# Performance work log

Hardware: AMD Instinct MI355X
Metric: run time of the kernel (lower is better)

Reference implementation:

```python
import jax, jax.numpy as jnp
import numpy as np

B, T, DIM, HEADS, DH = 4, 2048, 1024, 16, 64
MAX_SEQ_LEN = 2048


def setup_inputs() -> dict:
    key = jax.random.key(0)
    k1, k2, k3, k4 = jax.random.split(key, 4)
    x = jax.random.normal(k1, (B, T, DIM), dtype=jnp.float32)
    W_qkv = jax.random.normal(k2, (DIM, 3 * HEADS * DH), dtype=jnp.float32) * (DIM ** -0.5)
    W_0 = jax.random.normal(k3, (HEADS * DH, DIM), dtype=jnp.float32) * ((HEADS * DH) ** -0.5)
    rel_bias = jax.random.normal(k4, (2 * MAX_SEQ_LEN - 1, HEADS), dtype=jnp.float32) * 0.02
    return {"x": x, "W_qkv": W_qkv, "W_0": W_0, "rel_bias": rel_bias}


def reference(x, W_qkv, W_0, rel_bias):
    b, t, dim = x.shape
    heads = rel_bias.shape[1]
    dh = W_qkv.shape[1] // (3 * heads)
    scale = dh ** -0.5

    qkv = x @ W_qkv  # (b, t, 3*heads*dh), feature layout is (d, k, h): d slowest, h fastest
    qkv = qkv.reshape(b, t, dh, 3, heads)
    qkv = jnp.transpose(qkv, (3, 0, 4, 1, 2))  # (3, b, h, t, d)
    q, k, v = qkv[0], qkv[1], qkv[2]

    scores = jnp.einsum('bhid,bhjd->bhij', q, k) * scale  # (b, h, t, t)

    causal = jnp.tril(jnp.ones((t, t), dtype=bool))
    scores = jnp.where(causal[None, None], scores, -jnp.inf)

    # relative position bias: index = j - i + t - 1
    rel_idx = jnp.arange(t)[None, :] - jnp.arange(t)[:, None] + (t - 1)  # (t, t)
    bias = rel_bias[rel_idx]  # (t, t, heads)
    scores = scores + jnp.transpose(bias, (2, 0, 1))[None]

    attn = jax.nn.softmax(scores, axis=-1)
    out = jnp.einsum('bhij,bhjd->bhid', attn, v)  # (b, h, t, d)
    out = jnp.transpose(out, (0, 2, 1, 3)).reshape(b, t, heads * dh)
    return out @ W_0
```

## Files before the change

### kernel.cpp

```cpp
#include <hip/hip_runtime.h>
#include <hip/hip_bf16.h>
#include <stdint.h>

#define B_ 4
#define T_ 2048
#define NH 16
#define DH 64
#define DIM 1024
#define NF 3072
#define QKS 2048

typedef unsigned short u16;
typedef uint32_t u32;
typedef __bf16 bf16;
typedef bf16 bf16x8 __attribute__((ext_vector_type(8)));
typedef float f32x4 __attribute__((ext_vector_type(4)));
typedef u16 u16x8 __attribute__((ext_vector_type(8)));
typedef u16 u16x4 __attribute__((ext_vector_type(4)));

__device__ __forceinline__ u16 f2bf(float f) {
    u32 u = __builtin_bit_cast(u32, f);
    u = (u + 0x7fffu + ((u >> 16) & 1u)) >> 16;
    return (u16)u;
}

__device__ __forceinline__ float exp2f_fast(float x) {
#if __has_builtin(__builtin_amdgcn_exp2f)
    return __builtin_amdgcn_exp2f(x);
#else
    return exp2f(x);
#endif
}

#define GLOAD16(g, l)                                                          \
    __builtin_amdgcn_global_load_lds(                                          \
        (const __attribute__((address_space(1))) u32*)(g),                     \
        (__attribute__((address_space(3))) u32*)(l), 16, 0, 0)


__global__ __launch_bounds__(256) void cvt_bf16_k(const float* __restrict__ src,
                                                  u16* __restrict__ dst, int n8) {
    int i = blockIdx.x * 256 + threadIdx.x;
    if (i >= n8) return;
    const float4* s = (const float4*)src + (size_t)i * 2;
    float4 a = s[0], b = s[1];
    u16x8 o;
    o[0]=f2bf(a.x); o[1]=f2bf(a.y); o[2]=f2bf(a.z); o[3]=f2bf(a.w);
    o[4]=f2bf(b.x); o[5]=f2bf(b.y); o[6]=f2bf(b.z); o[7]=f2bf(b.w);
    *(u16x8*)(dst + (size_t)i * 8) = o;
}

template <int PERM>
__global__ __launch_bounds__(256) void wcvt_t_k(const float* __restrict__ src,
                                                u16* __restrict__ dst, int K, int N) {
    __shared__ float tile[32][33];
    int n0 = blockIdx.x * 32, k0 = blockIdx.y * 32;
    int c = threadIdx.x & 31, r0 = threadIdx.x >> 5;
#pragma unroll
    for (int i = 0; i < 4; i++) {
        int r = r0 + i * 8;
        tile[r][c] = src[(size_t)(k0 + r) * N + n0 + c];
    }
    __syncthreads();
#pragma unroll
    for (int i = 0; i < 4; i++) {
        int r = r0 + i * 8;
        int n = n0 + r;
        int nd;
        if (PERM) {
            int d = n / 48, rem = n - d * 48;
            int kk = rem >> 4, h = rem & 15;
            nd = kk * 1024 + h * 64 + d;
        } else {
            nd = n;
        }
        dst[(size_t)nd * K + k0 + c] = f2bf(tile[c][r]);
    }
}

__global__ __launch_bounds__(256) void rbt_k(const float* __restrict__ rb,
                                             u16* __restrict__ rbT2,
                                             u16* __restrict__ rbT2s) {
    int i = blockIdx.x * 256 + threadIdx.x;
    if (i >= NH * 4096) return;
    int h = i >> 12, d = i & 4095;
    float v = (d <= 2047) ? rb[(size_t)d * NH + h] * 1.44269504f : -1e30f;
    rbT2[i] = __builtin_bit_cast(u16, (bf16)v);
    int d2 = d + 1;
    float v2 = (d2 <= 2047) ? rb[(size_t)d2 * NH + h] * 1.44269504f : -1e30f;
    rbT2s[i] = __builtin_bit_cast(u16, (bf16)v2);
}


template <int OUTMODE>
__global__ __launch_bounds__(256, 2) void gemm_bt_k(const u16* __restrict__ A,
                                                    const u16* __restrict__ Bt,
                                                    void* __restrict__ Cout,
                                                    u16* __restrict__ Vt,
                                                    int M, int N, int K) {
    __shared__ __align__(16) u16 As[128 * 64];
    __shared__ __align__(16) u16 Bs[128 * 64];
    const int tid = threadIdx.x;
    const int wave = tid >> 6, lane = tid & 63;
    const int bm = blockIdx.x, bn = blockIdx.y;
    const int wr = (wave >> 1) * 64, wc = (wave & 1) * 64;
    const int lrow = lane & 15, g4 = lane >> 4;
    const int srow8 = lane >> 3;
    const int scs = (lane & 7) ^ srow8;
    const u16* Ab = A + (size_t)(bm * 128 + wave * 32) * K;
    const u16* Bb = Bt + (size_t)(bn * 128 + wave * 32) * K;
    u16* AsW = As + wave * 2048;
    u16* BsW = Bs + wave * 2048;
    const bool vt = (OUTMODE == 1) && (bn >= 16);
    f32x4 acc[4][4] = {};

    for (int k0 = 0; k0 < K; k0 += 64) {
        __syncthreads();
#pragma unroll
        for (int g = 0; g < 4; g++) {
            GLOAD16(Ab + (size_t)(g * 8 + srow8) * K + k0 + scs * 8, AsW + g * 512);
            GLOAD16(Bb + (size_t)(g * 8 + srow8) * K + k0 + scs * 8, BsW + g * 512);
        }
        __syncthreads();
#pragma unroll
        for (int kk2 = 0; kk2 < 2; kk2++) {
            bf16x8 af[4], bfr[4];
#pragma unroll
            for (int i = 0; i < 4; i++)
                af[i] = *(const bf16x8*)&As[(wr + i * 16 + lrow) * 64 +
                                            (((kk2 * 4 + g4) ^ (lrow & 7)) * 8)];
#pragma unroll
            for (int j = 0; j < 4; j++)
                bfr[j] = *(const bf16x8*)&Bs[(wc + j * 16 + lrow) * 64 +
                                             (((kk2 * 4 + g4) ^ (lrow & 7)) * 8)];
            if (vt) {
#pragma unroll
                for (int i = 0; i < 4; i++)
#pragma unroll
                    for (int j = 0; j < 4; j++)
                        acc[i][j] = __builtin_amdgcn_mfma_f32_16x16x32_bf16(
                            bfr[j], af[i], acc[i][j], 0, 0, 0);
            } else {
#pragma unroll
                for (int i = 0; i < 4; i++)
#pragma unroll
                    for (int j = 0; j < 4; j++)
                        acc[i][j] = __builtin_amdgcn_mfma_f32_16x16x32_bf16(
                            af[i], bfr[j], acc[i][j], 0, 0, 0);
            }
        }
    }

    const int crow = (lane >> 4) * 4, ccol = lane & 15;
    if (vt) {
#pragma unroll
        for (int i = 0; i < 4; i++)
#pragma unroll
            for (int j = 0; j < 4; j++) {
                int gm = bm * 128 + wr + i * 16 + ccol;
                int b = gm >> 11, tt = gm & 2047;
#pragma unroll
                for (int r = 0; r < 4; r++) {
                    int f = (bn - 16) * 128 + wc + j * 16 + crow + r;
                    int h = f >> 6, d = f & 63;
                    Vt[(((size_t)(b * NH + h)) * DH + d) * T_ + tt] =
                        f2bf(acc[i][j][r]);
                }
            }
    } else {
#pragma unroll
        for (int i = 0; i < 4; i++)
#pragma unroll
            for (int j = 0; j < 4; j++) {
                int gm = bm * 128 + wr + i * 16 + crow;
                int gn = bn * 128 + wc + j * 16 + ccol;
#pragma unroll
                for (int r = 0; r < 4; r++) {
                    if (OUTMODE == 1)
                        ((u16*)Cout)[(size_t)(gm + r) * N + gn] = f2bf(acc[i][j][r]);
                    else
                        ((float*)Cout)[(size_t)(gm + r) * N + gn] = acc[i][j][r];
                }
            }
    }
}

__global__ __launch_bounds__(256, 2) void flash_attn_k(const u16* __restrict__ qkF,
                                                       const u16* __restrict__ Vt,
                                                       const u16* __restrict__ rbT2,
                                                       const u16* __restrict__ rbT2s,
                                                       u16* __restrict__ O) {
    __shared__ __align__(16) u16 Ks[2][64 * 64];
    __shared__ __align__(16) u16 Vs[2][64 * 64];
    __shared__ __align__(16) u16 Ps[4][2][16 * 64];
    __shared__ __align__(16) u16 rbs2a[4096];
    __shared__ __align__(16) u16 rbs2b[4096];
    const int tid = threadIdx.x, wave = tid >> 6, lane = tid & 63;
    const int Lid = blockIdx.x;
    const int c = Lid & 7, u = Lid >> 3;
    const int bh = ((u & 7) << 3) | c;
    const int pair = u >> 3;
    const int h = bh & 15, b = bh >> 4;
    const int l15 = lane & 15, g4 = lane >> 4;
    const float SC2 = 0.125f * 1.44269504f;

    {
        *(u16x8*)&rbs2a[tid * 8] = *(const u16x8*)&rbT2[(size_t)h * 4096 + tid * 8];
        *(u16x8*)&rbs2a[2048 + tid * 8] = *(const u16x8*)&rbT2[(size_t)h * 4096 + 2048 + tid * 8];
        *(u16x8*)&rbs2b[tid * 8] = *(const u16x8*)&rbT2s[(size_t)h * 4096 + tid * 8];
        *(u16x8*)&rbs2b[2048 + tid * 8] = *(const u16x8*)&rbT2s[(size_t)h * 4096 + 2048 + tid * 8];
    }

    const size_t trow = (size_t)b * T_;
    u16* pwA = &Ps[wave][0][0];
    u16* pwB = &Ps[wave][1][0];
    const int lrow8 = lane >> 3, lch = lane & 7;
    const int swz = lch ^ lrow8;
    const u16* kg0 = &qkF[(trow + wave * 16 + lrow8) * QKS + 1024 + h * 64 + swz * 8];
    const u16* kg1 = kg0 + (size_t)8 * QKS;
    const u16* vg0 = &Vt[((size_t)bh * DH + wave * 16 + lrow8) * T_ + swz * 8];
    const u16* vg1 = vg0 + (size_t)8 * T_;

#define STAGE_KV(j0n, buf)                                                     \
    do {                                                                       \
        GLOAD16(kg0 + (size_t)(j0n) * QKS, &Ks[buf][(wave * 16) * 64]);        \
        GLOAD16(kg1 + (size_t)(j0n) * QKS, &Ks[buf][(wave * 16 + 8) * 64]);    \
        GLOAD16(vg0 + (j0n), &Vs[buf][(wave * 16) * 64]);                      \
        GLOAD16(vg1 + (j0n), &Vs[buf][(wave * 16 + 8) * 64]);                  \
    } while (0)

    STAGE_KV(0, 0);
    __syncthreads();
    int cur = 0;

    for (int half = 0; half < 2; half++) {
        const int blk = half ? 15 - pair : pair;
        const int qbA = blk * 128 + wave * 16;
        const int qbB = qbA + 64;
        bf16x8 aqA[2], aqB[2];
        aqA[0] = *(const bf16x8*)&qkF[(trow + qbA + l15) * QKS + h * 64 + g4 * 8];
        aqA[1] = *(const bf16x8*)&qkF[(trow + qbA + l15) * QKS + h * 64 + 32 + g4 * 8];
        aqB[0] = *(const bf16x8*)&qkF[(trow + qbB + l15) * QKS + h * 64 + g4 * 8];
        aqB[1] = *(const bf16x8*)&qkF[(trow + qbB + l15) * QKS + h * 64 + 32 + g4 * 8];

        const int ibA = 2047 - l15 + g4 * 4 - qbA;
        const u32* b32A = (const u32*)((ibA & 1) ? &rbs2b[ibA - 1] : &rbs2a[ibA]);
        const u32* b32B = b32A - 32;

        f32x4 oaccA[4] = {}, oaccB[4] = {};
        float lA = 0.f, lB = 0.f;

        const int jtmax = 2 * blk + 1;
        for (int jt = 0; jt <= jtmax; jt++) {
            const int j0 = jt * 64;
            const int j0n = (jt + 1 <= jtmax) ? (jt + 1) * 64 : (half == 0 ? 0 : -1);
            if (j0n >= 0) STAGE_KV(j0n, cur ^ 1);
            const u16* KsC = &Ks[cur][0];
            const u16* VsC = &Vs[cur][0];
            f32x4 sA[4], sB[4];
#pragma unroll
            for (int ni = 0; ni < 4; ni++) {
                f32x4 z = {};
                sA[ni] = z;
                sB[ni] = z;
            }
            __builtin_amdgcn_s_setprio(1);
#pragma unroll
            for (int ni = 0; ni < 4; ni++) {
                int arow = ni * 16 + l15;
#pragma unroll
                for (int kk = 0; kk < 2; kk++) {
                    int ch = kk * 4 + g4;
                    bf16x8 ak = *(const bf16x8*)&KsC[arow * 64 + ((ch ^ (arow & 7)) * 8)];
                    sA[ni] = __builtin_amdgcn_mfma_f32_16x16x32_bf16(ak, aqA[kk], sA[ni], 0, 0, 0);
                    sB[ni] = __builtin_amdgcn_mfma_f32_16x16x32_bf16(ak, aqB[kk], sB[ni], 0, 0, 0);
                }
            }
            __builtin_amdgcn_s_setprio(0);
            const int jo = j0 >> 1;
            {
                float su = 0.f;
#pragma unroll
                for (int ni = 0; ni < 4; ni++) {
                    u32 w0 = b32A[jo + ni * 8];
                    u32 w1 = b32A[jo + ni * 8 + 1];
                    float e0 = exp2f_fast(fmaf(sA[ni][0], SC2, __builtin_bit_cast(float, w0 << 16)));
                    float e1 = exp2f_fast(fmaf(sA[ni][1], SC2, __builtin_bit_cast(float, w0 & 0xffff0000u)));
                    float e2 = exp2f_fast(fmaf(sA[ni][2], SC2, __builtin_bit_cast(float, w1 << 16)));
                    float e3 = exp2f_fast(fmaf(sA[ni][3], SC2, __builtin_bit_cast(float, w1 & 0xffff0000u)));
                    su += (e0 + e1) + (e2 + e3);
                    u16x4 pk;
                    pk[0] = __builtin_bit_cast(u16, (bf16)e0);
                    pk[1] = __builtin_bit_cast(u16, (bf16)e1);
                    pk[2] = __builtin_bit_cast(u16, (bf16)e2);
                    pk[3] = __builtin_bit_cast(u16, (bf16)e3);
                    int colb = ni * 16 + g4 * 4;
                    int ch = colb >> 3, co = colb & 7;
                    *(u16x4*)&pwA[l15 * 64 + ((ch ^ (l15 & 7)) * 8) + co] = pk;
                }
                su += __shfl_xor(su, 16);
                su += __shfl_xor(su, 32);
                lA += su;
            }
            {
                float su = 0.f;
#pragma unroll
                for (int ni = 0; ni < 4; ni++) {
                    u32 w0 = b32B[jo + ni * 8];
                    u32 w1 = b32B[jo + ni * 8 + 1];
                    float e0 = exp2f_fast(fmaf(sB[ni][0], SC2, __builtin_bit_cast(float, w0 << 16)));
                    float e1 = exp2f_fast(fmaf(sB[ni][1], SC2, __builtin_bit_cast(float, w0 & 0xffff0000u)));
                    float e2 = exp2f_fast(fmaf(sB[ni][2], SC2, __builtin_bit_cast(float, w1 << 16)));
                    float e3 = exp2f_fast(fmaf(sB[ni][3], SC2, __builtin_bit_cast(float, w1 & 0xffff0000u)));
                    su += (e0 + e1) + (e2 + e3);
                    u16x4 pk;
                    pk[0] = __builtin_bit_cast(u16, (bf16)e0);
                    pk[1] = __builtin_bit_cast(u16, (bf16)e1);
                    pk[2] = __builtin_bit_cast(u16, (bf16)e2);
                    pk[3] = __builtin_bit_cast(u16, (bf16)e3);
                    int colb = ni * 16 + g4 * 4;
                    int ch = colb >> 3, co = colb & 7;
                    *(u16x4*)&pwB[l15 * 64 + ((ch ^ (l15 & 7)) * 8) + co] = pk;
                }
                su += __shfl_xor(su, 16);
                su += __shfl_xor(su, 32);
                lB += su;
            }
            bf16x8 bpA[2], bpB[2];
#pragma unroll
            for (int kk = 0; kk < 2; kk++) {
                int ch = kk * 4 + g4;
                int off = l15 * 64 + ((ch ^ (l15 & 7)) * 8);
                bpA[kk] = *(const bf16x8*)&pwA[off];
                bpB[kk] = *(const bf16x8*)&pwB[off];
            }
            __builtin_amdgcn_s_setprio(1);
#pragma unroll
            for (int di = 0; di < 4; di++) {
                int vrow = di * 16 + l15;
#pragma unroll
                for (int kk = 0; kk < 2; kk++) {
                    int ch = kk * 4 + g4;
                    bf16x8 av = *(const bf16x8*)&VsC[vrow * 64 + ((ch ^ (vrow & 7)) * 8)];
                    oaccA[di] = __builtin_amdgcn_mfma_f32_16x16x32_bf16(av, bpA[kk], oaccA[di], 0, 0, 0);
                    oaccB[di] = __builtin_amdgcn_mfma_f32_16x16x32_bf16(av, bpB[kk], oaccB[di], 0, 0, 0);
                }
            }
            __builtin_amdgcn_s_setprio(0);
            __syncthreads();
            cur ^= 1;
        }
        {
            float inv = 1.0f / lA;
            u16* orow = &O[((size_t)b * T_ + qbA + l15) * (NH * DH) + h * DH];
#pragma unroll
            for (int di = 0; di < 4; di++) {
                u16x4 ov;
#pragma unroll
                for (int r = 0; r < 4; r++)
                    ov[r] = __builtin_bit_cast(u16, (bf16)(oaccA[di][r] * inv));
                *(u16x4*)&orow[di * 16 + g4 * 4] = ov;
            }
        }
        {
            float inv = 1.0f / lB;
            u16* orow = &O[((size_t)b * T_ + qbB + l15) * (NH * DH) + h * DH];
#pragma unroll
            for (int di = 0; di < 4; di++) {
                u16x4 ov;
#pragma unroll
                for (int r = 0; r < 4; r++)
                    ov[r] = __builtin_bit_cast(u16, (bf16)(oaccB[di][r] * inv));
                *(u16x4*)&orow[di * 16 + g4 * 4] = ov;
            }
        }
    }
#undef STAGE_KV
}


extern "C" void kernel_launch(void* const* d_in, const int* in_sizes, int n_in,
                              void* d_out, int out_size, void* d_ws, size_t ws_size,
                              hipStream_t stream) {
    const float* x    = (const float*)d_in[0];
    const float* Wqkv = (const float*)d_in[1];
    const float* W0   = (const float*)d_in[2];
    const float* rb   = (const float*)d_in[3];
    char* ws = (char*)d_ws;

    u16*   xb    = (u16*)(ws + 0);
    u16*   WqkvT = (u16*)(ws + 16777216);
    u16*   W0T   = (u16*)(ws + 23068672);
    u16*   rbT2  = (u16*)(ws + 25165824);
    u16*   rbT2s = (u16*)(ws + 25296896);
    u16*   qkF   = (u16*)(ws + 25427968);
    u16*   attnO = (u16*)(ws + 58982400);
    u16*   Vtb   = (u16*)(ws + 75759616);

    cvt_bf16_k<<<4096, 256, 0, stream>>>(x, xb, (B_ * T_ * DIM) / 8);
    wcvt_t_k<1><<<dim3(NF / 32, DIM / 32), 256, 0, stream>>>(Wqkv, WqkvT, DIM, NF);
    wcvt_t_k<0><<<dim3(DIM / 32, DIM / 32), 256, 0, stream>>>(W0, W0T, DIM, DIM);
    rbt_k<<<(NH * 4096 + 255) / 256, 256, 0, stream>>>(rb, rbT2, rbT2s);

    gemm_bt_k<1><<<dim3((B_ * T_) / 128, NF / 128), 256, 0, stream>>>(
        xb, WqkvT, qkF, Vtb, B_ * T_, QKS, DIM);

    flash_attn_k<<<512, 256, 0, stream>>>(qkF, Vtb, rbT2, rbT2s, attnO);

    gemm_bt_k<0><<<dim3((B_ * T_) / 128, DIM / 128), 256, 0, stream>>>(
        attnO, W0T, d_out, nullptr, B_ * T_, DIM, DIM);
}
```

Baseline: 167.8 us.

## Fuse x bf16 conversion into QKV GEMM and merge prep kernels

Removes the separate x-to-bf16 conversion pass: the QKV GEMM now reads fp32 x directly, converts it in registers and writes the swizzled bf16 tile into shared memory. The weight transpose/convert kernels and the relative-bias kernel are merged into one launch. This saves a full write and re-read of a 16MB intermediate plus several launches. In exchange, A-tile loads in the GEMM become synchronous register loads instead of async global-to-LDS copies, and the fp32 x is re-read once per N-block (24 times), which doubles the A traffic into the GEMM.

```diff
diff --git a/kernel.cpp b/kernel.cpp
--- a/kernel.cpp
+++ b/kernel.cpp
@@ -37,63 +37,58 @@
         (const __attribute__((address_space(1))) u32*)(g),                     \
         (__attribute__((address_space(3))) u32*)(l), 16, 0, 0)
 
-
-__global__ __launch_bounds__(256) void cvt_bf16_k(const float* __restrict__ src,
-                                                  u16* __restrict__ dst, int n8) {
-    int i = blockIdx.x * 256 + threadIdx.x;
-    if (i >= n8) return;
-    const float4* s = (const float4*)src + (size_t)i * 2;
-    float4 a = s[0], b = s[1];
-    u16x8 o;
-    o[0]=f2bf(a.x); o[1]=f2bf(a.y); o[2]=f2bf(a.z); o[3]=f2bf(a.w);
-    o[4]=f2bf(b.x); o[5]=f2bf(b.y); o[6]=f2bf(b.z); o[7]=f2bf(b.w);
-    *(u16x8*)(dst + (size_t)i * 8) = o;
-}
-
-template <int PERM>
-__global__ __launch_bounds__(256) void wcvt_t_k(const float* __restrict__ src,
-                                                u16* __restrict__ dst, int K, int N) {
+__global__ __launch_bounds__(256) void prep_k(const float* __restrict__ Wqkv,
+                                              const float* __restrict__ W0,
+                                              const float* __restrict__ rb,
+                                              u16* __restrict__ WqkvT,
+                                              u16* __restrict__ W0T,
+                                              u16* __restrict__ rbT2,
+                                              u16* __restrict__ rbT2s) {
     __shared__ float tile[32][33];
-    int n0 = blockIdx.x * 32, k0 = blockIdx.y * 32;
-    int c = threadIdx.x & 31, r0 = threadIdx.x >> 5;
-#pragma unroll
-    for (int i = 0; i < 4; i++) {
-        int r = r0 + i * 8;
-        tile[r][c] = src[(size_t)(k0 + r) * N + n0 + c];
+    const int bid = blockIdx.x;
+    if (bid < 4096) {
+        const bool perm = bid < 3072;
+        const float* src = perm ? Wqkv : W0;
+        u16* dst = perm ? WqkvT : W0T;
+        const int N = perm ? NF : DIM;
+        const int r2 = perm ? bid : bid - 3072;
+        const int nb = perm ? 96 : 32;
+        const int n0 = (r2 % nb) * 32, k0 = (r2 / nb) * 32;
+        int c = threadIdx.x & 31, r0 = threadIdx.x >> 5;
+#pragma unroll
+        for (int i = 0; i < 4; i++) {
+            int r = r0 + i * 8;
+            tile[r][c] = src[(size_t)(k0 + r) * N + n0 + c];
+        }
+        __syncthreads();
+#pragma unroll
+        for (int i = 0; i < 4; i++) {
+            int r = r0 + i * 8;
+            int n = n0 + r;
+            int nd;
+            if (perm) {
+                int d = n / 48, rem = n - d * 48;
+                int kk = rem >> 4, h = rem & 15;
+                nd = kk * 1024 + h * 64 + d;
+            } else {
+                nd = n;
+            }
+            dst[(size_t)nd * DIM + k0 + c] = f2bf(tile[c][r]);
+        }
+    } else {
+        int i = (bid - 4096) * 256 + threadIdx.x;
+        int h = i >> 12, d = i & 4095;
+        float v = (d <= 2047) ? rb[(size_t)d * NH + h] * 1.44269504f : -1e30f;
+        rbT2[i] = __builtin_bit_cast(u16, (bf16)v);
+        int d2 = d + 1;
+        float v2 = (d2 <= 2047) ? rb[(size_t)d2 * NH + h] * 1.44269504f : -1e30f;
+        rbT2s[i] = __builtin_bit_cast(u16, (bf16)v2);
     }
-    __syncthreads();
-#pragma unroll
-    for (int i = 0; i < 4; i++) {
-        int r = r0 + i * 8;
-        int n = n0 + r;
-        int nd;
-        if (PERM) {
-            int d = n / 48, rem = n - d * 48;
-            int kk = rem >> 4, h = rem & 15;
-            nd = kk * 1024 + h * 64 + d;
-        } else {
-            nd = n;
-        }
-        dst[(size_t)nd * K + k0 + c] = f2bf(tile[c][r]);
-    }
-}
-
-__global__ __launch_bounds__(256) void rbt_k(const float* __restrict__ rb,
-                                             u16* __restrict__ rbT2,
-                                             u16* __restrict__ rbT2s) {
-    int i = blockIdx.x * 256 + threadIdx.x;
-    if (i >= NH * 4096) return;
-    int h = i >> 12, d = i & 4095;
-    float v = (d <= 2047) ? rb[(size_t)d * NH + h] * 1.44269504f : -1e30f;
-    rbT2[i] = __builtin_bit_cast(u16, (bf16)v);
-    int d2 = d + 1;
-    float v2 = (d2 <= 2047) ? rb[(size_t)d2 * NH + h] * 1.44269504f : -1e30f;
-    rbT2s[i] = __builtin_bit_cast(u16, (bf16)v2);
 }
 
 
 template <int OUTMODE>
-__global__ __launch_bounds__(256, 2) void gemm_bt_k(const u16* __restrict__ A,
+__global__ __launch_bounds__(256, 2) void gemm_bt_k(const void* __restrict__ A,
                                                     const u16* __restrict__ Bt,
                                                     void* __restrict__ Cout,
                                                     u16* __restrict__ Vt,
@@ -107,7 +102,10 @@
     const int lrow = lane & 15, g4 = lane >> 4;
     const int srow8 = lane >> 3;
     const int scs = (lane & 7) ^ srow8;
-    const u16* Ab = A + (size_t)(bm * 128 + wave * 32) * K;
+    const u16* Ab = (OUTMODE == 0)
+        ? (const u16*)A + (size_t)(bm * 128 + wave * 32) * K : nullptr;
+    const float* Af = (OUTMODE == 1)
+        ? (const float*)A + (size_t)(bm * 128 + wave * 32 + srow8) * K : nullptr;
     const u16* Bb = Bt + (size_t)(bn * 128 + wave * 32) * K;
     u16* AsW = As + wave * 2048;
     u16* BsW = Bs + wave * 2048;
@@ -117,9 +115,33 @@
     for (int k0 = 0; k0 < K; k0 += 64) {
         __syncthreads();
 #pragma unroll
-        for (int g = 0; g < 4; g++) {
-            GLOAD16(Ab + (size_t)(g * 8 + srow8) * K + k0 + scs * 8, AsW + g * 512);
+        for (int g = 0; g < 4; g++)
             GLOAD16(Bb + (size_t)(g * 8 + srow8) * K + k0 + scs * 8, BsW + g * 512);
+        if (OUTMODE == 1) {
+            float4 f0[4], f1[4];
+#pragma unroll
+            for (int g = 0; g < 4; g++) {
+                const float* ap = &Af[(size_t)(g * 8) * K + k0 + scs * 8];
+                f0[g] = *(const float4*)ap;
+                f1[g] = *(const float4*)(ap + 4);
+            }
+#pragma unroll
+            for (int g = 0; g < 4; g++) {
+                u16x8 o;
+                o[0] = __builtin_bit_cast(u16, (bf16)f0[g].x);
+                o[1] = __builtin_bit_cast(u16, (bf16)f0[g].y);
+                o[2] = __builtin_bit_cast(u16, (bf16)f0[g].z);
+                o[3] = __builtin_bit_cast(u16, (bf16)f0[g].w);
+                o[4] = __builtin_bit_cast(u16, (bf16)f1[g].x);
+                o[5] = __builtin_bit_cast(u16, (bf16)f1[g].y);
+                o[6] = __builtin_bit_cast(u16, (bf16)f1[g].z);
+                o[7] = __builtin_bit_cast(u16, (bf16)f1[g].w);
+                *(u16x8*)&AsW[g * 512 + lane * 8] = o;
+            }
+        } else {
+#pragma unroll
+            for (int g = 0; g < 4; g++)
+                GLOAD16(Ab + (size_t)(g * 8 + srow8) * K + k0 + scs * 8, AsW + g * 512);
         }
         __syncthreads();
 #pragma unroll
@@ -388,22 +410,18 @@
     const float* rb   = (const float*)d_in[3];
     char* ws = (char*)d_ws;
 
-    u16*   xb    = (u16*)(ws + 0);
-    u16*   WqkvT = (u16*)(ws + 16777216);
-    u16*   W0T   = (u16*)(ws + 23068672);
-    u16*   rbT2  = (u16*)(ws + 25165824);
-    u16*   rbT2s = (u16*)(ws + 25296896);
-    u16*   qkF   = (u16*)(ws + 25427968);
-    u16*   attnO = (u16*)(ws + 58982400);
-    u16*   Vtb   = (u16*)(ws + 75759616);
-
-    cvt_bf16_k<<<4096, 256, 0, stream>>>(x, xb, (B_ * T_ * DIM) / 8);
-    wcvt_t_k<1><<<dim3(NF / 32, DIM / 32), 256, 0, stream>>>(Wqkv, WqkvT, DIM, NF);
-    wcvt_t_k<0><<<dim3(DIM / 32, DIM / 32), 256, 0, stream>>>(W0, W0T, DIM, DIM);
-    rbt_k<<<(NH * 4096 + 255) / 256, 256, 0, stream>>>(rb, rbT2, rbT2s);
+    u16*   WqkvT = (u16*)(ws + 0);
+    u16*   W0T   = (u16*)(ws + 6291456);
+    u16*   rbT2  = (u16*)(ws + 8388608);
+    u16*   rbT2s = (u16*)(ws + 8519680);
+    u16*   qkF   = (u16*)(ws + 8650752);
+    u16*   attnO = (u16*)(ws + 42205184);
+    u16*   Vtb   = (u16*)(ws + 58982400);
+
+    prep_k<<<4352, 256, 0, stream>>>(Wqkv, W0, rb, WqkvT, W0T, rbT2, rbT2s);
 
     gemm_bt_k<1><<<dim3((B_ * T_) / 128, NF / 128), 256, 0, stream>>>(
-        xb, WqkvT, qkF, Vtb, B_ * T_, QKS, DIM);
+        x, WqkvT, qkF, Vtb, B_ * T_, QKS, DIM);
 
     flash_attn_k<<<512, 256, 0, stream>>>(qkF, Vtb, rbT2, rbT2s, attnO);
 
```

Result: slower. 173.9 us (+3.6%).
